# Optimization experiments

Measured on AMD Instinct MI355X. Metric: run time of the kernel, lower is better.

The kernel has to match this reference:

```python
import jax, jax.numpy as jnp
import numpy as np
from jax import lax

B, PN, NS = 8, 16384, 256
KDIM, HID = 512, 384
HALF = HID // 2
EPS = 1e-5


def setup_inputs() -> dict:
    key = jax.random.key(0)
    ks = jax.random.split(key, 12)
    s = lambda fan: np.float32(1.0 / np.sqrt(fan))
    inp = {
        "p": jax.random.normal(ks[0], (B, PN, 3), jnp.float32),
        "N": NS,
        "patch_feature": jax.random.normal(ks[1], (B, KDIM, 1), jnp.float32),
        # Linear(k_dim, hidden)
        "W_feat": jax.random.normal(ks[2], (KDIM, HID), jnp.float32) * s(KDIM),
        "b_feat": jax.random.normal(ks[3], (HID,), jnp.float32) * s(KDIM),
        # Linear(3, hidden//2)
        "W_coord": jax.random.normal(ks[4], (3, HALF), jnp.float32) * s(3),
        "b_coord": jax.random.normal(ks[5], (HALF,), jnp.float32) * s(3),
        # Conv1d(hidden+hidden//2, hidden, 1) == per-point linear, weight (out,in)
        "W1": jax.random.normal(ks[6], (HID, HID + HALF), jnp.float32) * s(HID + HALF),
        "b1": jax.random.normal(ks[7], (HID,), jnp.float32) * s(HID + HALF),
        "g1": jnp.ones((HID,), jnp.float32),
        "be1": jnp.zeros((HID,), jnp.float32),
        # Conv1d(hidden, hidden, 1)
        "W2": jax.random.normal(ks[8], (HID, HID), jnp.float32) * s(HID),
        "b2": jax.random.normal(ks[9], (HID,), jnp.float32) * s(HID),
        "g2": jnp.ones((HID,), jnp.float32),
        "be2": jnp.zeros((HID,), jnp.float32),
    }
    return inp


def farthest_point_sample(points, k):
    """points: (B, N, C) -> (B, k, C). Deterministic start index 0 per batch."""
    b, n, c = points.shape

    def step(carry, _):
        dist, far = carry
        centroid = jnp.take_along_axis(points, far[:, None, None], axis=1)  # (B,1,C)
        d = jnp.sum((points - centroid) ** 2, axis=-1)                      # (B,N)
        dist = jnp.minimum(dist, d)
        new_far = jnp.argmax(dist, axis=-1)
        return (dist, new_far), far

    init = (jnp.full((b, n), 1e10, points.dtype), jnp.zeros((b,), jnp.int32))
    _, idx = lax.scan(step, init, None, length=k)  # idx: (k, B)
    idx = idx.T                                    # (B, k)
    return jnp.take_along_axis(points, idx[:, :, None], axis=1)  # (B,k,C)


def batchnorm(x, gamma, beta):
    """x: (B, L, C); training-mode BN over (B, L) per channel (biased var)."""
    mean = jnp.mean(x, axis=(0, 1))
    var = jnp.var(x, axis=(0, 1))
    return (x - mean) * lax.rsqrt(var + EPS) * gamma + beta


def reference(p, N, patch_feature, W_feat, b_feat, W_coord, b_coord,
              W1, b1, g1, be1, W2, b2, g2, be2):
    b, pn, _ = p.shape
    global_feat = patch_feature[..., 0] @ W_feat + b_feat          # (B, HID)
    global_feat = jnp.broadcast_to(global_feat[:, None, :], (b, N, HID))
    local_feat = p @ W_coord + b_coord                              # (B, PN, HALF)
    if N != pn:
        local_feat = farthest_point_sample(local_feat, N)           # (B, N, HALF)
    combined = jnp.concatenate([global_feat, local_feat], axis=-1)  # (B, N, HID+HALF)
    h = jnp.einsum("bnc,oc->bno", combined, W1) + b1
    h = jax.nn.relu(batchnorm(h, g1, be1))
    h = jnp.einsum("bnc,oc->bno", h, W2) + b2
    h = jax.nn.relu(batchnorm(h, g2, be2))
    return h  # (B, N, HID)
```

## Files before the change

kernel.cpp:

```cpp
#include <hip/hip_runtime.h>

#define BATCH 8
#define PN    16384
#define NSAMP 256
#define KDIM  512
#define HID   384
#define HALF  192
#define CIN   576
#define ROWS  2048
#define BN_EPS 1e-5f

#define OFF_GF   0
#define OFF_W1T  3072
#define OFF_GFW  76800
#define OFF_W2T  224256
#define OFF_IDX  371712
#define OFF_H1   373760
#define OFF_H2   1160192
#define OFF_SUM1 1946624
#define OFF_SQ1  1947008
#define OFF_SUM2 1947392
#define OFF_SQ2  1947776

typedef float v2f __attribute__((ext_vector_type(2)));

__global__ __launch_bounds__(1024) void k_main(const float* p, const float* Wc,
                                               const float* pf, const float* Wf,
                                               const float* bfe, const float* W1,
                                               const float* b1v, const float* W2,
                                               float* ws) {
  __shared__ float s[KDIM];
  __shared__ float Msh[6];
  __shared__ __align__(16) float redv[2][16];
  __shared__ __align__(16) float4 cslot[2][8];
  __shared__ int widx[2], ncl[2];
  int blk = blockIdx.x, t = threadIdx.x;

  if (blk >= 8) {
    if (blk < 16) {
      for (int sI = (blk - 8) * 1024 + t; sI < HID * HALF; sI += 8192) {
        int o = sI / HALF, c = sI % HALF;
        ws[OFF_W1T + c * HID + o] = W1[o * CIN + HID + c];
      }
    } else if (blk < 24) {
      for (int sI = (blk - 16) * 1024 + t; sI < HID * HID; sI += 8192) {
        int o = sI / HID, c = sI % HID;
        ws[OFF_W2T + c * HID + o] = W2[sI];
      }
    } else if (blk < 32) {
      int b = blk - 24;
      if (t < KDIM) s[t] = pf[b * KDIM + t];
      __syncthreads();
      float acc = 0.f;
      if (t < HID) {
        acc = bfe[t];
        for (int k = 0; k < KDIM; k++) acc = fmaf(s[k], Wf[k * HID + t], acc);
        ws[OFF_GF + b * HID + t] = acc;
      }
      __syncthreads();
      if (t < HID) s[t] = acc;
      __syncthreads();
      if (t < HID) {
        float g = b1v[t];
        const float* w1row = W1 + t * CIN;
        for (int c = 0; c < HID; c++) g = fmaf(s[c], w1row[c], g);
        ws[OFF_GFW + b * HID + t] = g;
      }
    } else {
      for (int i = t; i < 1536; i += 1024) ws[OFF_SUM1 + i] = 0.f;
    }
    return;
  }

  int b = blk;
  int* idx_out = (int*)(ws + OFF_IDX);

  if (t < 64) {
    double g0 = 0, g1 = 0, g2 = 0, g3 = 0, g4 = 0, g5 = 0;
    for (int k = t; k < HALF; k += 64) {
      double w0 = (double)Wc[k];
      double w1 = (double)Wc[HALF + k];
      double w2 = (double)Wc[2 * HALF + k];
      g0 += w0 * w0; g1 += w0 * w1; g2 += w0 * w2;
      g3 += w1 * w1; g4 += w1 * w2; g5 += w2 * w2;
    }
    for (int off = 32; off; off >>= 1) {
      g0 += __shfl_down(g0, off, 64); g1 += __shfl_down(g1, off, 64);
      g2 += __shfl_down(g2, off, 64); g3 += __shfl_down(g3, off, 64);
      g4 += __shfl_down(g4, off, 64); g5 += __shfl_down(g5, off, 64);
    }
    if (t == 0) {
      double l00 = sqrt(g0);
      double l10 = g1 / l00, l20 = g2 / l00;
      double l11 = sqrt(g3 - l10 * l10);
      double l21 = (g4 - l10 * l20) / l11;
      double l22 = sqrt(g5 - l20 * l20 - l21 * l21);
      Msh[0] = (float)l00; Msh[1] = (float)l10; Msh[2] = (float)l20;
      Msh[3] = (float)l11; Msh[4] = (float)l21; Msh[5] = (float)l22;
    }
  }
  __syncthreads();
  float m00 = Msh[0], m10 = Msh[1], m20 = Msh[2];
  float m11 = Msh[3], m21 = Msh[4], m22 = Msh[5];

  const float* pb = p + b * PN * 3;
  v2f qx[8], qy[8], qz[8], nq[8], dist[8];
#pragma unroll
  for (int j = 0; j < 8; j++) {
    int i0 = ((2 * j) << 10) + t;
    int i1 = i0 + 1024;
    float x0 = pb[i0 * 3], y0 = pb[i0 * 3 + 1], z0 = pb[i0 * 3 + 2];
    float x1 = pb[i1 * 3], y1 = pb[i1 * 3 + 1], z1 = pb[i1 * 3 + 2];
    qx[j] = (v2f){fmaf(m00, x0, fmaf(m10, y0, m20 * z0)),
                  fmaf(m00, x1, fmaf(m10, y1, m20 * z1))};
    qy[j] = (v2f){fmaf(m11, y0, m21 * z0), fmaf(m11, y1, m21 * z1)};
    qz[j] = (v2f){m22 * z0, m22 * z1};
    nq[j] = __builtin_elementwise_fma(
        qx[j], qx[j],
        __builtin_elementwise_fma(qy[j], qy[j], qz[j] * qz[j]));
    dist[j] = (v2f){1e10f, 1e10f};
  }

  if (t == 0) {
    widx[1] = 0; ncl[1] = 1;
    cslot[1][0] = make_float4(__int_as_float(0), qx[0].x, qy[0].x, qz[0].x);
    widx[0] = 0x7fffffff; ncl[0] = 0;
  }
  __syncthreads();

  int par = 0;
  for (int k = 0; k < NSAMP; k++) {
    int qb = par ^ 1;
    int far = widx[qb];
    float4 s0 = cslot[qb][0];
    float cx = s0.y, cy = s0.z, cz = s0.w;
    if (__float_as_int(s0.x) != far) {
      int n = ncl[qb];
      bool found = false;
      int nn = n < 8 ? n : 8;
      for (int i2 = 1; i2 < nn; i2++) {
        float4 si = cslot[qb][i2];
        if (__float_as_int(si.x) == far) {
          cx = si.y; cy = si.z; cz = si.w; found = true;
        }
      }
      if (!found) {
        float x = pb[far * 3], y = pb[far * 3 + 1], z = pb[far * 3 + 2];
        cx = fmaf(m00, x, fmaf(m10, y, m20 * z));
        cy = fmaf(m11, y, m21 * z);
        cz = m22 * z;
      }
    }
    if (t == 0) {
      idx_out[b * NSAMP + k] = far;
      widx[par] = 0x7fffffff;
      ncl[par] = 0;
    }

    float nc = fmaf(cx, cx, fmaf(cy, cy, cz * cz));
    float cx2 = -2.f * cx, cy2 = -2.f * cy, cz2 = -2.f * cz;
    v2f cxv = (v2f){cx2, cx2}, cyv = (v2f){cy2, cy2}, czv = (v2f){cz2, cz2};
    v2f ncv = (v2f){nc, nc};
#pragma unroll
    for (int j = 0; j < 8; j++) {
      v2f base = nq[j] + ncv;
      v2f d = __builtin_elementwise_fma(
          qx[j], cxv,
          __builtin_elementwise_fma(qy[j], cyv,
              __builtin_elementwise_fma(qz[j], czv, base)));
      dist[j].x = fminf(dist[j].x, d.x);
      dist[j].y = fminf(dist[j].y, d.y);
    }
    float a0 = fmaxf(dist[0].x, dist[0].y);
    float a1 = fmaxf(dist[1].x, dist[1].y);
    float a2 = fmaxf(dist[2].x, dist[2].y);
    float a3 = fmaxf(dist[3].x, dist[3].y);
    float a4 = fmaxf(dist[4].x, dist[4].y);
    float a5 = fmaxf(dist[5].x, dist[5].y);
    float a6 = fmaxf(dist[6].x, dist[6].y);
    float a7 = fmaxf(dist[7].x, dist[7].y);
    float b0 = fmaxf(fmaxf(a0, a1), a2);
    float b1 = fmaxf(fmaxf(a3, a4), a5);
    float tmax = fmaxf(fmaxf(b0, b1), fmaxf(a6, a7));
    float m = tmax;
#pragma unroll
    for (int off = 32; off; off >>= 1) m = fmaxf(m, __shfl_xor(m, off, 64));
    if ((t & 63) == 0) redv[par][t >> 6] = m;
    __syncthreads();
    float4 r0 = *(const float4*)&redv[par][0];
    float4 r1 = *(const float4*)&redv[par][4];
    float4 r2 = *(const float4*)&redv[par][8];
    float4 r3 = *(const float4*)&redv[par][12];
    float g01 = fmaxf(fmaxf(r0.x, r0.y), r0.z);
    float g02 = fmaxf(fmaxf(r0.w, r1.x), r1.y);
    float g03 = fmaxf(fmaxf(r1.z, r1.w), r2.x);
    float g04 = fmaxf(fmaxf(r2.y, r2.z), r2.w);
    float g05 = fmaxf(fmaxf(r3.x, r3.y), r3.z);
    float gmax = fmaxf(fmaxf(fmaxf(g01, g02), g03),
                       fmaxf(fmaxf(g04, g05), r3.w));
    if (tmax == gmax) {
      int mi = 0x7fffffff; float wx = 0.f, wy = 0.f, wz = 0.f;
#pragma unroll
      for (int j = 7; j >= 0; j--) {
        int i0 = ((2 * j) << 10) + t;
        bool hy = (dist[j].y == gmax);
        mi = hy ? i0 + 1024 : mi;
        wx = hy ? qx[j].y : wx; wy = hy ? qy[j].y : wy; wz = hy ? qz[j].y : wz;
        bool hx = (dist[j].x == gmax);
        mi = hx ? i0 : mi;
        wx = hx ? qx[j].x : wx; wy = hx ? qy[j].x : wy; wz = hx ? qz[j].x : wz;
      }
      int pos = atomicAdd(&ncl[par], 1);
      if (pos < 8)
        cslot[par][pos] = make_float4(__int_as_float(mi), wx, wy, wz);
      atomicMin(&widx[par], mi);
    }
    __syncthreads();
    par ^= 1;
  }
}

__global__ __launch_bounds__(384) void k_gemm1(const float* p,
                                               const float* Wc,
                                               const float* bc,
                                               float* ws) {
  __shared__ __align__(16) float ct[HALF * 8];
  int t = threadIdx.x;
  int row0 = blockIdx.x * 8;
  int b = row0 >> 8;
  const int* fidx = (const int*)(ws + OFF_IDX);
  for (int sI = t; sI < 8 * HALF; sI += 384) {
    int r = sI / HALF, co = sI % HALF;
    int row = row0 + r;
    int i = fidx[row];
    const float* pp = p + (b * PN + i) * 3;
    float val = bc[co];
    val = fmaf(pp[0], Wc[co], val);
    val = fmaf(pp[1], Wc[HALF + co], val);
    val = fmaf(pp[2], Wc[2 * HALF + co], val);
    ct[co * 8 + r] = val;
  }
  __syncthreads();
  const float* w1t = ws + OFF_W1T;
  float acc[8] = {0.f, 0.f, 0.f, 0.f, 0.f, 0.f, 0.f, 0.f};
  for (int c = 0; c < HALF; c++) {
    float w = w1t[c * HID + t];
    float4 a0 = *(const float4*)(ct + c * 8);
    float4 a1 = *(const float4*)(ct + c * 8 + 4);
    acc[0] = fmaf(a0.x, w, acc[0]); acc[1] = fmaf(a0.y, w, acc[1]);
    acc[2] = fmaf(a0.z, w, acc[2]); acc[3] = fmaf(a0.w, w, acc[3]);
    acc[4] = fmaf(a1.x, w, acc[4]); acc[5] = fmaf(a1.y, w, acc[5]);
    acc[6] = fmaf(a1.z, w, acc[6]); acc[7] = fmaf(a1.w, w, acc[7]);
  }
  float base = ws[OFF_GFW + b * HID + t];
  float sv = 0.f, sq = 0.f;
#pragma unroll
  for (int r = 0; r < 8; r++) {
    float v = acc[r] + base;
    ws[OFF_H1 + (row0 + r) * HID + t] = v;
    sv += v; sq = fmaf(v, v, sq);
  }
  atomicAdd(&ws[OFF_SUM1 + t], sv);
  atomicAdd(&ws[OFF_SQ1 + t], sq);
}

__global__ __launch_bounds__(384) void k_gemm2(const float* b2,
                                               const float* g1,
                                               const float* be1,
                                               float* ws) {
  __shared__ __align__(16) float ht[HID * 8];
  __shared__ float sc1s[HID], sh1s[HID];
  int t = threadIdx.x;
  int row0 = blockIdx.x * 8;
  {
    float m = ws[OFF_SUM1 + t] * (1.f / ROWS);
    float v = ws[OFF_SQ1 + t] * (1.f / ROWS) - m * m;
    float inv = 1.f / sqrtf(v + BN_EPS);
    float sc = inv * g1[t];
    sc1s[t] = sc;
    sh1s[t] = be1[t] - m * sc;
  }
  __syncthreads();
  for (int sI = t; sI < 8 * HID; sI += 384) {
    int r = sI / HID, c = sI % HID;
    float x = fmaf(ws[OFF_H1 + (row0 + r) * HID + c], sc1s[c], sh1s[c]);
    ht[c * 8 + r] = fmaxf(x, 0.f);
  }
  __syncthreads();
  const float* w2t = ws + OFF_W2T;
  float acc[8] = {0.f, 0.f, 0.f, 0.f, 0.f, 0.f, 0.f, 0.f};
  for (int c = 0; c < HID; c++) {
    float w = w2t[c * HID + t];
    float4 a0 = *(const float4*)(ht + c * 8);
    float4 a1 = *(const float4*)(ht + c * 8 + 4);
    acc[0] = fmaf(a0.x, w, acc[0]); acc[1] = fmaf(a0.y, w, acc[1]);
    acc[2] = fmaf(a0.z, w, acc[2]); acc[3] = fmaf(a0.w, w, acc[3]);
    acc[4] = fmaf(a1.x, w, acc[4]); acc[5] = fmaf(a1.y, w, acc[5]);
    acc[6] = fmaf(a1.z, w, acc[6]); acc[7] = fmaf(a1.w, w, acc[7]);
  }
  float bias = b2[t];
  float sv = 0.f, sq = 0.f;
#pragma unroll
  for (int r = 0; r < 8; r++) {
    float v = acc[r] + bias;
    ws[OFF_H2 + (row0 + r) * HID + t] = v;
    sv += v; sq = fmaf(v, v, sq);
  }
  atomicAdd(&ws[OFF_SUM2 + t], sv);
  atomicAdd(&ws[OFF_SQ2 + t], sq);
}

__global__ __launch_bounds__(256) void k_out(const float* ws, const float* g2,
                                             const float* be2, float* out) {
  int gid = blockIdx.x * 256 + threadIdx.x;
  int i = gid * 4;
  int c = i % HID;
  float4 h  = *(const float4*)(ws + OFF_H2 + i);
  float4 s2 = *(const float4*)(ws + OFF_SUM2 + c);
  float4 q2 = *(const float4*)(ws + OFF_SQ2 + c);
  float4 gv = *(const float4*)(g2 + c);
  float4 bv = *(const float4*)(be2 + c);
  float4 r;
#define BN2(comp) {                                                  \
    float m  = s2.comp * (1.f / ROWS);                               \
    float v  = q2.comp * (1.f / ROWS) - m * m;                       \
    float sc = (1.f / sqrtf(v + BN_EPS)) * gv.comp;                  \
    float sh = bv.comp - m * sc;                                     \
    r.comp = fmaxf(fmaf(h.comp, sc, sh), 0.f); }
  BN2(x) BN2(y) BN2(z) BN2(w)
#undef BN2
  ((float4*)out)[gid] = r;
}

extern "C" void kernel_launch(void* const* d_in, const int* in_sizes, int n_in,
                              void* d_out, int out_size, void* d_ws, size_t ws_size,
                              hipStream_t stream) {
  const float* p   = (const float*)d_in[0];
  const float* pf  = (const float*)d_in[2];
  const float* Wf  = (const float*)d_in[3];
  const float* bfe = (const float*)d_in[4];
  const float* Wc  = (const float*)d_in[5];
  const float* bc  = (const float*)d_in[6];
  const float* W1  = (const float*)d_in[7];
  const float* b1  = (const float*)d_in[8];
  const float* g1  = (const float*)d_in[9];
  const float* be1 = (const float*)d_in[10];
  const float* W2  = (const float*)d_in[11];
  const float* b2  = (const float*)d_in[12];
  const float* g2  = (const float*)d_in[13];
  const float* be2 = (const float*)d_in[14];
  float* ws = (float*)d_ws;

  hipLaunchKernelGGL(k_main,  dim3(33),  dim3(1024), 0, stream,
                     p, Wc, pf, Wf, bfe, W1, b1, W2, ws);
  hipLaunchKernelGGL(k_gemm1, dim3(256), dim3(384), 0, stream, p, Wc, bc, ws);
  hipLaunchKernelGGL(k_gemm2, dim3(256), dim3(384), 0, stream, b2, g1, be1, ws);
  hipLaunchKernelGGL(k_out,   dim3(768), dim3(256), 0, stream,
                     ws, g2, be2, (float*)d_out);
}
```

Measured before the change: 512.8 us.

## Halve FPS block size, store transformed points in workspace for centroid lookup

The farthest-point-sampling kernel now runs 512 threads per batch instead of 1024, so each thread holds 32 points in registers. This halves the cross-wave reduction width (8 waves instead of 16). The shared-memory candidate slot cache with its fallback global recompute is removed. Instead, all transformed points plus their norms are written once to a float4 scratch region in the H1 workspace, and the chosen centroid is read from there each iteration. The max reduction is vectorised with packed min/max. The trade-offs are a per-iteration global load on the serial critical path and higher register pressure, and the scratch region reuses the H1 buffer before gemm1 writes it.

```diff
diff --git a/kernel.cpp b/kernel.cpp
--- a/kernel.cpp
+++ b/kernel.cpp
@@ -24,26 +24,25 @@
 
 typedef float v2f __attribute__((ext_vector_type(2)));
 
-__global__ __launch_bounds__(1024) void k_main(const float* p, const float* Wc,
-                                               const float* pf, const float* Wf,
-                                               const float* bfe, const float* W1,
-                                               const float* b1v, const float* W2,
-                                               float* ws) {
+__global__ __launch_bounds__(512, 2) void k_main(const float* p, const float* Wc,
+                                                 const float* pf, const float* Wf,
+                                                 const float* bfe, const float* W1,
+                                                 const float* b1v, const float* W2,
+                                                 float* ws) {
   __shared__ float s[KDIM];
   __shared__ float Msh[6];
-  __shared__ __align__(16) float redv[2][16];
-  __shared__ __align__(16) float4 cslot[2][8];
-  __shared__ int widx[2], ncl[2];
+  __shared__ __align__(16) float redv[2][8];
+  __shared__ int widx[2];
   int blk = blockIdx.x, t = threadIdx.x;
 
   if (blk >= 8) {
     if (blk < 16) {
-      for (int sI = (blk - 8) * 1024 + t; sI < HID * HALF; sI += 8192) {
+      for (int sI = (blk - 8) * 512 + t; sI < HID * HALF; sI += 4096) {
         int o = sI / HALF, c = sI % HALF;
         ws[OFF_W1T + c * HID + o] = W1[o * CIN + HID + c];
       }
     } else if (blk < 24) {
-      for (int sI = (blk - 16) * 1024 + t; sI < HID * HID; sI += 8192) {
+      for (int sI = (blk - 16) * 512 + t; sI < HID * HID; sI += 4096) {
         int o = sI / HID, c = sI % HID;
         ws[OFF_W2T + c * HID + o] = W2[sI];
       }
@@ -67,7 +66,7 @@
         ws[OFF_GFW + b * HID + t] = g;
       }
     } else {
-      for (int i = t; i < 1536; i += 1024) ws[OFF_SUM1 + i] = 0.f;
+      for (int i = t; i < 1536; i += 512) ws[OFF_SUM1 + i] = 0.f;
     }
     return;
   }
@@ -104,11 +103,12 @@
   float m11 = Msh[3], m21 = Msh[4], m22 = Msh[5];
 
   const float* pb = p + b * PN * 3;
-  v2f qx[8], qy[8], qz[8], nq[8], dist[8];
-#pragma unroll
-  for (int j = 0; j < 8; j++) {
-    int i0 = ((2 * j) << 10) + t;
-    int i1 = i0 + 1024;
+  float4* qws = (float4*)(ws + OFF_H1) + b * PN;
+  v2f qx[16], qy[16], qz[16], nq[16], dist[16];
+#pragma unroll
+  for (int j = 0; j < 16; j++) {
+    int i0 = (j << 10) + t;
+    int i1 = i0 + 512;
     float x0 = pb[i0 * 3], y0 = pb[i0 * 3 + 1], z0 = pb[i0 * 3 + 2];
     float x1 = pb[i1 * 3], y1 = pb[i1 * 3 + 1], z1 = pb[i1 * 3 + 2];
     qx[j] = (v2f){fmaf(m00, x0, fmaf(m10, y0, m20 * z0)),
@@ -119,69 +119,49 @@
         qx[j], qx[j],
         __builtin_elementwise_fma(qy[j], qy[j], qz[j] * qz[j]));
     dist[j] = (v2f){1e10f, 1e10f};
-  }
-
-  if (t == 0) {
-    widx[1] = 0; ncl[1] = 1;
-    cslot[1][0] = make_float4(__int_as_float(0), qx[0].x, qy[0].x, qz[0].x);
-    widx[0] = 0x7fffffff; ncl[0] = 0;
-  }
+    qws[i0] = make_float4(qx[j].x, qy[j].x, qz[j].x, nq[j].x);
+    qws[i1] = make_float4(qx[j].y, qy[j].y, qz[j].y, nq[j].y);
+  }
+
+  if (t == 0) { widx[1] = 0; widx[0] = 0x7fffffff; }
   __syncthreads();
 
   int par = 0;
   for (int k = 0; k < NSAMP; k++) {
-    int qb = par ^ 1;
-    int far = widx[qb];
-    float4 s0 = cslot[qb][0];
-    float cx = s0.y, cy = s0.z, cz = s0.w;
-    if (__float_as_int(s0.x) != far) {
-      int n = ncl[qb];
-      bool found = false;
-      int nn = n < 8 ? n : 8;
-      for (int i2 = 1; i2 < nn; i2++) {
-        float4 si = cslot[qb][i2];
-        if (__float_as_int(si.x) == far) {
-          cx = si.y; cy = si.z; cz = si.w; found = true;
-        }
-      }
-      if (!found) {
-        float x = pb[far * 3], y = pb[far * 3 + 1], z = pb[far * 3 + 2];
-        cx = fmaf(m00, x, fmaf(m10, y, m20 * z));
-        cy = fmaf(m11, y, m21 * z);
-        cz = m22 * z;
-      }
-    }
+    int far = widx[par ^ 1];
     if (t == 0) {
       idx_out[b * NSAMP + k] = far;
       widx[par] = 0x7fffffff;
-      ncl[par] = 0;
-    }
-
-    float nc = fmaf(cx, cx, fmaf(cy, cy, cz * cz));
-    float cx2 = -2.f * cx, cy2 = -2.f * cy, cz2 = -2.f * cz;
+    }
+    float4 qc = qws[far];
+    float cx2 = -2.f * qc.x, cy2 = -2.f * qc.y, cz2 = -2.f * qc.z;
     v2f cxv = (v2f){cx2, cx2}, cyv = (v2f){cy2, cy2}, czv = (v2f){cz2, cz2};
-    v2f ncv = (v2f){nc, nc};
-#pragma unroll
-    for (int j = 0; j < 8; j++) {
+    v2f ncv = (v2f){qc.w, qc.w};
+#pragma unroll
+    for (int j = 0; j < 16; j++) {
       v2f base = nq[j] + ncv;
       v2f d = __builtin_elementwise_fma(
           qx[j], cxv,
           __builtin_elementwise_fma(qy[j], cyv,
               __builtin_elementwise_fma(qz[j], czv, base)));
-      dist[j].x = fminf(dist[j].x, d.x);
-      dist[j].y = fminf(dist[j].y, d.y);
-    }
-    float a0 = fmaxf(dist[0].x, dist[0].y);
-    float a1 = fmaxf(dist[1].x, dist[1].y);
-    float a2 = fmaxf(dist[2].x, dist[2].y);
-    float a3 = fmaxf(dist[3].x, dist[3].y);
-    float a4 = fmaxf(dist[4].x, dist[4].y);
-    float a5 = fmaxf(dist[5].x, dist[5].y);
-    float a6 = fmaxf(dist[6].x, dist[6].y);
-    float a7 = fmaxf(dist[7].x, dist[7].y);
-    float b0 = fmaxf(fmaxf(a0, a1), a2);
-    float b1 = fmaxf(fmaxf(a3, a4), a5);
-    float tmax = fmaxf(fmaxf(b0, b1), fmaxf(a6, a7));
+      dist[j] = __builtin_elementwise_min(dist[j], d);
+    }
+    v2f t0v = __builtin_elementwise_max(dist[0], dist[1]);
+    v2f t1v = __builtin_elementwise_max(dist[2], dist[3]);
+    v2f t2v = __builtin_elementwise_max(dist[4], dist[5]);
+    v2f t3v = __builtin_elementwise_max(dist[6], dist[7]);
+    v2f t4v = __builtin_elementwise_max(dist[8], dist[9]);
+    v2f t5v = __builtin_elementwise_max(dist[10], dist[11]);
+    v2f t6v = __builtin_elementwise_max(dist[12], dist[13]);
+    v2f t7v = __builtin_elementwise_max(dist[14], dist[15]);
+    t0v = __builtin_elementwise_max(t0v, t1v);
+    t2v = __builtin_elementwise_max(t2v, t3v);
+    t4v = __builtin_elementwise_max(t4v, t5v);
+    t6v = __builtin_elementwise_max(t6v, t7v);
+    t0v = __builtin_elementwise_max(t0v, t2v);
+    t4v = __builtin_elementwise_max(t4v, t6v);
+    t0v = __builtin_elementwise_max(t0v, t4v);
+    float tmax = fmaxf(t0v.x, t0v.y);
     float m = tmax;
 #pragma unroll
     for (int off = 32; off; off >>= 1) m = fmaxf(m, __shfl_xor(m, off, 64));
@@ -189,30 +169,17 @@
     __syncthreads();
     float4 r0 = *(const float4*)&redv[par][0];
     float4 r1 = *(const float4*)&redv[par][4];
-    float4 r2 = *(const float4*)&redv[par][8];
-    float4 r3 = *(const float4*)&redv[par][12];
-    float g01 = fmaxf(fmaxf(r0.x, r0.y), r0.z);
-    float g02 = fmaxf(fmaxf(r0.w, r1.x), r1.y);
-    float g03 = fmaxf(fmaxf(r1.z, r1.w), r2.x);
-    float g04 = fmaxf(fmaxf(r2.y, r2.z), r2.w);
-    float g05 = fmaxf(fmaxf(r3.x, r3.y), r3.z);
-    float gmax = fmaxf(fmaxf(fmaxf(g01, g02), g03),
-                       fmaxf(fmaxf(g04, g05), r3.w));
+    float g01 = fmaxf(fmaxf(r0.x, r0.y), fmaxf(r0.z, r0.w));
+    float g02 = fmaxf(fmaxf(r1.x, r1.y), fmaxf(r1.z, r1.w));
+    float gmax = fmaxf(g01, g02);
     if (tmax == gmax) {
-      int mi = 0x7fffffff; float wx = 0.f, wy = 0.f, wz = 0.f;
-#pragma unroll
-      for (int j = 7; j >= 0; j--) {
-        int i0 = ((2 * j) << 10) + t;
-        bool hy = (dist[j].y == gmax);
-        mi = hy ? i0 + 1024 : mi;
-        wx = hy ? qx[j].y : wx; wy = hy ? qy[j].y : wy; wz = hy ? qz[j].y : wz;
-        bool hx = (dist[j].x == gmax);
-        mi = hx ? i0 : mi;
-        wx = hx ? qx[j].x : wx; wy = hx ? qy[j].x : wy; wz = hx ? qz[j].x : wz;
-      }
-      int pos = atomicAdd(&ncl[par], 1);
-      if (pos < 8)
-        cslot[par][pos] = make_float4(__int_as_float(mi), wx, wy, wz);
+      int mi = 0x7fffffff;
+#pragma unroll
+      for (int j = 15; j >= 0; j--) {
+        int i0 = (j << 10) + t;
+        mi = (dist[j].y == gmax) ? i0 + 512 : mi;
+        mi = (dist[j].x == gmax) ? i0 : mi;
+      }
       atomicMin(&widx[par], mi);
     }
     __syncthreads();
@@ -351,7 +318,7 @@
   const float* be2 = (const float*)d_in[14];
   float* ws = (float*)d_ws;
 
-  hipLaunchKernelGGL(k_main,  dim3(33),  dim3(1024), 0, stream,
+  hipLaunchKernelGGL(k_main,  dim3(33),  dim3(512), 0, stream,
                      p, Wc, pf, Wf, bfe, W1, b1, W2, ws);
   hipLaunchKernelGGL(k_gemm1, dim3(256), dim3(384), 0, stream, p, Wc, bc, ws);
   hipLaunchKernelGGL(k_gemm2, dim3(256), dim3(384), 0, stream, b2, g1, be1, ws);
```

Measured after the change: 526.3 us. +2.6%, slower.
